# Kernel tuning notes

Measured on AMD Instinct MI355X. Metric: run time of the kernel, lower is better.

Reference implementation:

```python
import jax, jax.numpy as jnp
import numpy as np

NUM_CAPSULE = 16
DIM_CAPSULE = 64
ROUTINGS = 3
T_EPS = 1e-7


def setup_inputs() -> dict:
    key = jax.random.key(0)
    k1, k2 = jax.random.split(key)
    x = jax.random.normal(k1, (64, 512, 768), dtype=jnp.float32)
    # xavier-normal-ish init for W: [1, input_dim_capsule, num_capsule*dim_capsule]
    fan_in, fan_out = 768, NUM_CAPSULE * DIM_CAPSULE
    std = float(np.sqrt(2.0 / (fan_in + fan_out)))
    W = jax.random.normal(k2, (1, 768, NUM_CAPSULE * DIM_CAPSULE), dtype=jnp.float32) * std
    return {"x": x, "W": W}


def _squash(v, eps=T_EPS):
    # NOTE: this module's 'squash' is pure L2 normalization with eps, not the
    # classic (s^2/(1+s^2)) squash.
    s2 = jnp.sum(v * v, axis=-1, keepdims=True)
    return v / jnp.sqrt(s2 + eps)


def reference(x, W):
    B, In, _ = x.shape
    # u_hat: [B, In, num*dim] -> [B, num, In, dim]
    u = jnp.matmul(x, W).reshape(B, In, NUM_CAPSULE, DIM_CAPSULE).transpose(0, 2, 1, 3)
    b = jnp.zeros((B, NUM_CAPSULE, In), dtype=u.dtype)  # routing logits
    outputs = None
    for i in range(ROUTINGS):
        # torch code softmaxes over the num_capsule axis (after permute dance)
        c = jax.nn.softmax(b, axis=1)  # [B, num, In]
        outputs = _squash(jnp.einsum('bij,bijk->bik', c, u))  # [B, num, dim]
        if i < ROUTINGS - 1:
            b = jnp.einsum('bik,bijk->bij', outputs, u)  # [B, num, In]
    return outputs
```

## Files before the change

kernel.cpp:

```cpp
#include <hip/hip_runtime.h>
#include <hip/hip_bf16.h>
#include <stdint.h>

#define BATCH 64
#define IN_CAPS 512
#define NCAP 16
#define DCAP 64
#define GN (NCAP * DCAP)
#define GM (BATCH * IN_CAPS)
#define GK 768

typedef __bf16 bf16;
typedef __attribute__((ext_vector_type(8))) __bf16 bf16x8;
typedef __attribute__((ext_vector_type(4))) float f32x4;

__device__ inline void async16(const bf16* g, bf16* l) {
    __builtin_amdgcn_global_load_lds(
        (__attribute__((address_space(1))) void*)g,
        (__attribute__((address_space(3))) void*)l, 16, 0, 0);
}

__global__ __launch_bounds__(256) void k_convX2(const float* __restrict__ X,
                                                bf16* __restrict__ Xb,
                                                float* __restrict__ XS) {
    __shared__ float ls[GK];
    const int tid = threadIdx.x;
    ls[tid] = 0.f; ls[tid + 256] = 0.f; ls[tid + 512] = 0.f;
    __syncthreads();
    const size_t base = (size_t)blockIdx.x * (32 * GK);
    float acc[3][8] = {};
#pragma unroll
    for (int r = 0; r < 12; ++r) {
        const int off = r * 2048 + tid * 8;
        const f32x4 a0 = *(const f32x4*)(X + base + off);
        const f32x4 a1 = *(const f32x4*)(X + base + off + 4);
        bf16x8 o;
        o[0] = (bf16)a0[0]; o[1] = (bf16)a0[1]; o[2] = (bf16)a0[2]; o[3] = (bf16)a0[3];
        o[4] = (bf16)a1[0]; o[5] = (bf16)a1[1]; o[6] = (bf16)a1[2]; o[7] = (bf16)a1[3];
        *(bf16x8*)(Xb + base + off) = o;
        const int g = r % 3;
        acc[g][0] += a0[0]; acc[g][1] += a0[1];
        acc[g][2] += a0[2]; acc[g][3] += a0[3];
        acc[g][4] += a1[0]; acc[g][5] += a1[1];
        acc[g][6] += a1[2]; acc[g][7] += a1[3];
    }
    if (XS != nullptr) {
#pragma unroll
        for (int g = 0; g < 3; ++g) {
            const int cg = (g == 1) ? 512 : (g == 2) ? 256 : 0;
            const int kb = (tid * 8 + cg) % GK;
#pragma unroll
            for (int j = 0; j < 8; ++j) atomicAdd(&ls[kb + j], acc[g][j]);
        }
        __syncthreads();
        const int bidx = blockIdx.x >> 4;
        atomicAdd(&XS[(size_t)bidx * GK + tid],       ls[tid]);
        atomicAdd(&XS[(size_t)bidx * GK + tid + 256], ls[tid + 256]);
        atomicAdd(&XS[(size_t)bidx * GK + tid + 512], ls[tid + 512]);
    }
}

__global__ void k_transW(const float* __restrict__ W, bf16* __restrict__ Wt,
                         float* __restrict__ XS) {
    __shared__ bf16 t[32][33];
    const int k0 = blockIdx.x * 32;
    const int n0 = blockIdx.y * 32;
    const int tx = threadIdx.x, ty = threadIdx.y;
    if (XS != nullptr) {
        const int gid = (blockIdx.y * gridDim.x + blockIdx.x) * 256 + ty * 32 + tx;
        if (gid < BATCH * GK) XS[gid] = 0.f;
    }
#pragma unroll
    for (int r = 0; r < 4; ++r)
        t[ty + r * 8][tx] = (bf16)W[(size_t)(k0 + ty + r * 8) * GN + n0 + tx];
    __syncthreads();
#pragma unroll
    for (int r = 0; r < 4; ++r)
        Wt[(size_t)(n0 + ty + r * 8) * GK + k0 + tx] = t[tx][ty + r * 8];
}

__global__ __launch_bounds__(256) void k_out1(const float* __restrict__ XS,
                                              const float* __restrict__ W,
                                              float* __restrict__ O1) {
    __shared__ float xs[4][GK];
    __shared__ float red[4][4][64];
    const int cap = blockIdx.x & 15;
    const int bg = blockIdx.x >> 4;
    const int tid = threadIdx.x;
    const int k = tid & 63, kq = tid >> 6;
#pragma unroll
    for (int bb = 0; bb < 4; ++bb) {
        const size_t b = (size_t)(bg * 4 + bb);
        xs[bb][tid]       = XS[b * GK + tid];
        xs[bb][tid + 256] = XS[b * GK + tid + 256];
        xs[bb][tid + 512] = XS[b * GK + tid + 512];
    }
    __syncthreads();
    float acc4[4] = {0.f, 0.f, 0.f, 0.f};
    const float* wp = W + (size_t)(kq * 192) * GN + cap * 64 + k;
#pragma unroll 4
    for (int kk = 0; kk < 192; ++kk) {
        const float w = wp[(size_t)kk * GN];
        const int kx = kq * 192 + kk;
        acc4[0] += xs[0][kx] * w;
        acc4[1] += xs[1][kx] * w;
        acc4[2] += xs[2][kx] * w;
        acc4[3] += xs[3][kx] * w;
    }
#pragma unroll
    for (int bb = 0; bb < 4; ++bb) red[bb][kq][k] = acc4[bb];
    __syncthreads();
    if (tid < 64) {
#pragma unroll
        for (int bb = 0; bb < 4; ++bb) {
            float s = (red[bb][0][tid] + red[bb][1][tid] +
                       red[bb][2][tid] + red[bb][3][tid]) * 0.0625f;
            float ss = s * s;
#pragma unroll
            for (int off = 32; off >= 1; off >>= 1) ss += __shfl_xor(ss, off);
            O1[((size_t)(bg * 4 + bb) * NCAP + cap) * DCAP + tid] =
                s * rsqrtf(ss + 1e-7f);
        }
    }
}

__global__ __launch_bounds__(256) void k_gemm_pipe(const bf16* __restrict__ Xb,
                                                   const bf16* __restrict__ Wt,
                                                   const float* __restrict__ O1,
                                                   bf16* __restrict__ U,
                                                   float* __restrict__ BL) {
    __shared__ bf16 sA[3 * 4096];
    __shared__ bf16 sB[3 * 4096];

    const int tid = threadIdx.x;
    const int lane = tid & 63;
    const int wave = tid >> 6;
    const int wm = wave >> 1, wn = wave & 1;
    const int m0 = blockIdx.x * 128;
    const int n0 = blockIdx.y * 128;

    const int r16 = lane & 15, q8 = (lane >> 4) * 8;
    const bf16* gA0 = Xb + (size_t)(m0 + wave * 16 + r16) * GK + q8;
    const bf16* gA1 = Xb + (size_t)(m0 + (wave + 4) * 16 + r16) * GK + q8;
    const bf16* gB0 = Wt + (size_t)(n0 + wave * 16 + r16) * GK + q8;
    const bf16* gB1 = Wt + (size_t)(n0 + (wave + 4) * 16 + r16) * GK + q8;

    f32x4 acc[4][4] = {};

#define STAGE(BUF) do {                                        \
        async16(gA0, sA + (BUF) * 4096 + wave * 512);          \
        async16(gA1, sA + (BUF) * 4096 + (wave + 4) * 512);    \
        async16(gB0, sB + (BUF) * 4096 + wave * 512);          \
        async16(gB1, sB + (BUF) * 4096 + (wave + 4) * 512);    \
        gA0 += 32; gA1 += 32; gB0 += 32; gB1 += 32;            \
    } while (0)

    auto gstep = [&](int buf) {
        bf16x8 af[4], bv[4];
#pragma unroll
        for (int mi = 0; mi < 4; ++mi)
            af[mi] = *(const bf16x8*)(sA + buf * 4096 + (wm * 4 + mi) * 512 + lane * 8);
#pragma unroll
        for (int ni = 0; ni < 4; ++ni)
            bv[ni] = *(const bf16x8*)(sB + buf * 4096 + (wn * 4 + ni) * 512 + lane * 8);
#pragma unroll
        for (int mi = 0; mi < 4; ++mi)
#pragma unroll
            for (int ni = 0; ni < 4; ++ni)
                acc[mi][ni] = __builtin_amdgcn_mfma_f32_16x16x32_bf16(
                    af[mi], bv[ni], acc[mi][ni], 0, 0, 0);
    };

    STAGE(0);
    STAGE(1);

    int cur = 0, nxt = 2;
    for (int kt = 0; kt < GK / 32 - 2; ++kt) {
        asm volatile("s_waitcnt lgkmcnt(0)" ::: "memory");
        asm volatile("s_waitcnt vmcnt(4)" ::: "memory");
        __builtin_amdgcn_s_barrier();
        __builtin_amdgcn_sched_barrier(0);
        STAGE(nxt);
        gstep(cur);
        cur = (cur == 2) ? 0 : cur + 1;
        nxt = (nxt == 2) ? 0 : nxt + 1;
    }
    asm volatile("s_waitcnt lgkmcnt(0)" ::: "memory");
    asm volatile("s_waitcnt vmcnt(4)" ::: "memory");
    __builtin_amdgcn_s_barrier();
    __builtin_amdgcn_sched_barrier(0);
    gstep(1);
    asm volatile("s_waitcnt lgkmcnt(0)" ::: "memory");
    asm volatile("s_waitcnt vmcnt(0)" ::: "memory");
    __builtin_amdgcn_s_barrier();
    __builtin_amdgcn_sched_barrier(0);
    gstep(2);
#undef STAGE

    const int fr = lane & 15;
    const int fq = lane >> 4;
#pragma unroll
    for (int mi = 0; mi < 4; ++mi) {
#pragma unroll
        for (int ni = 0; ni < 4; ++ni) {
#pragma unroll
            for (int r = 0; r < 4; ++r) {
                const int m = m0 + wm * 64 + mi * 16 + fq * 4 + r;
                const int n = n0 + wn * 64 + ni * 16 + fr;
                const int bb = m >> 9, j = m & 511;
                const int ci = n >> 6, k = n & 63;
                U[(((size_t)(bb * NCAP + ci)) * IN_CAPS + j) * DCAP + k] =
                    (bf16)acc[mi][ni][r];
            }
        }
    }

    if (O1 != nullptr) {
        const int b = m0 >> 9;
        const int cap = (n0 >> 6) + wn;
        float o1v[4];
#pragma unroll
        for (int ni = 0; ni < 4; ++ni)
            o1v[ni] = O1[(size_t)b * GN + n0 + wn * 64 + ni * 16 + fr];
#pragma unroll
        for (int mi = 0; mi < 4; ++mi) {
#pragma unroll
            for (int r = 0; r < 4; ++r) {
                float p = o1v[0] * acc[mi][0][r] + o1v[1] * acc[mi][1][r] +
                          o1v[2] * acc[mi][2][r] + o1v[3] * acc[mi][3][r];
                p += __shfl_xor(p, 1);
                p += __shfl_xor(p, 2);
                p += __shfl_xor(p, 4);
                p += __shfl_xor(p, 8);
                if (fr == 0) {
                    const int j = (m0 & 511) + wm * 64 + mi * 16 + fq * 4 + r;
                    BL[((size_t)(b * NCAP + cap)) * IN_CAPS + j] = p;
                }
            }
        }
    }
}

__global__ __launch_bounds__(256) void k_gemm_inline(const float* __restrict__ X,
                                                     const bf16* __restrict__ Wt,
                                                     bf16* __restrict__ U) {
    __shared__ bf16 sA[128 * 32];
    __shared__ bf16 sB[128 * 32];
    const int tid = threadIdx.x;
    const int lane = tid & 63;
    const int wave = tid >> 6;
    const int wm = wave >> 1, wn = wave & 1;
    const int m0 = blockIdx.x * 128;
    const int n0 = blockIdx.y * 128;
    const int srow = tid >> 2;
    const int scol = (tid & 3) * 8;
    f32x4 acc[4][4] = {};
    const int fr = lane & 15;
    const int fq = lane >> 4;
    for (int kt = 0; kt < GK / 32; ++kt) {
        const int kb = kt * 32;
        bf16x8 a0, a1, b0, b1;
        {
            const float* p = X + (size_t)(m0 + srow) * GK + kb + scol;
            const f32x4 x0 = *(const f32x4*)p, x1 = *(const f32x4*)(p + 4);
            const float* q = X + (size_t)(m0 + srow + 64) * GK + kb + scol;
            const f32x4 y0 = *(const f32x4*)q, y1 = *(const f32x4*)(q + 4);
#pragma unroll
            for (int c = 0; c < 4; ++c) {
                a0[c] = (bf16)x0[c]; a0[c + 4] = (bf16)x1[c];
                a1[c] = (bf16)y0[c]; a1[c + 4] = (bf16)y1[c];
            }
        }
        b0 = *(const bf16x8*)(Wt + (size_t)(n0 + srow) * GK + kb + scol);
        b1 = *(const bf16x8*)(Wt + (size_t)(n0 + srow + 64) * GK + kb + scol);
        __syncthreads();
        *(bf16x8*)(sA + srow * 32 + scol) = a0;
        *(bf16x8*)(sA + (srow + 64) * 32 + scol) = a1;
        *(bf16x8*)(sB + srow * 32 + scol) = b0;
        *(bf16x8*)(sB + (srow + 64) * 32 + scol) = b1;
        __syncthreads();
        bf16x8 af[4], bfr[4];
#pragma unroll
        for (int mi = 0; mi < 4; ++mi)
            af[mi] = *(const bf16x8*)(sA + (wm * 64 + mi * 16 + fr) * 32 + fq * 8);
#pragma unroll
        for (int ni = 0; ni < 4; ++ni)
            bfr[ni] = *(const bf16x8*)(sB + (wn * 64 + ni * 16 + fr) * 32 + fq * 8);
#pragma unroll
        for (int mi = 0; mi < 4; ++mi)
#pragma unroll
            for (int ni = 0; ni < 4; ++ni)
                acc[mi][ni] = __builtin_amdgcn_mfma_f32_16x16x32_bf16(
                    af[mi], bfr[ni], acc[mi][ni], 0, 0, 0);
    }
#pragma unroll
    for (int mi = 0; mi < 4; ++mi) {
#pragma unroll
        for (int ni = 0; ni < 4; ++ni) {
#pragma unroll
            for (int r = 0; r < 4; ++r) {
                const int m = m0 + wm * 64 + mi * 16 + fq * 4 + r;
                const int n = n0 + wn * 64 + ni * 16 + fr;
                const int bb = m >> 9, j = m & 511;
                const int ci = n >> 6, k = n & 63;
                U[(((size_t)(bb * NCAP + ci)) * IN_CAPS + j) * DCAP + k] =
                    (bf16)acc[mi][ni][r];
            }
        }
    }
}

__global__ __launch_bounds__(256) void k_route(const bf16* __restrict__ U,
                                               float* __restrict__ BL,
                                               float* __restrict__ OutC,
                                               int mode) {
    __shared__ float sc[IN_CAPS];
    __shared__ float red[32][64];
    __shared__ float sout[64];
    const int bi = blockIdx.x;
    const int b = bi >> 4, cap = bi & 15;
    const int tid = threadIdx.x;
    const size_t ubase = (size_t)bi * IN_CAPS * DCAP;

    if (mode == 0) {
        sc[tid] = 0.0625f;
        sc[tid + 256] = 0.0625f;
    } else {
#pragma unroll
        for (int h = 0; h < 2; ++h) {
            const int j = tid + h * 256;
            const float* p = BL + (size_t)b * NCAP * IN_CAPS + j;
            float v[16], mx = -1e30f;
#pragma unroll
            for (int i = 0; i < 16; ++i) {
                v[i] = p[(size_t)i * IN_CAPS];
                mx = fmaxf(mx, v[i]);
            }
            float s = 0.f;
#pragma unroll
            for (int i = 0; i < 16; ++i) s += __expf(v[i] - mx);
            sc[j] = __expf(v[cap] - mx) / s;
        }
    }
    __syncthreads();

    const int g = tid & 7;
    const int jr = tid >> 3;

    float acc[8] = {};
#pragma unroll
    for (int it = 0; it < 16; ++it) {
        const int j = it * 32 + jr;
        const bf16x8 v = *(const bf16x8*)(U + ubase + (size_t)it * 2048 + tid * 8);
        const float cv = sc[j];
#pragma unroll
        for (int c = 0; c < 8; ++c) acc[c] += cv * (float)v[c];
    }
    *(f32x4*)(&red[jr][g * 8]) = f32x4{acc[0], acc[1], acc[2], acc[3]};
    *(f32x4*)(&red[jr][g * 8 + 4]) = f32x4{acc[4], acc[5], acc[6], acc[7]};
    __syncthreads();

    if (tid < 64) {
        float s = 0.f;
#pragma unroll
        for (int r = 0; r < 32; ++r) s += red[r][tid];
        float ss = s * s;
#pragma unroll
        for (int off = 32; off >= 1; off >>= 1) ss += __shfl_xor(ss, off);
        const float val = s * rsqrtf(ss + 1e-7f);
        sout[tid] = val;
        if (mode == 2) OutC[(size_t)bi * DCAP + tid] = val;
    }
    if (mode == 2) return;
    __syncthreads();

    const f32x4 o0 = *(const f32x4*)(sout + g * 8);
    const f32x4 o1 = *(const f32x4*)(sout + g * 8 + 4);
#pragma unroll
    for (int it = 0; it < 16; ++it) {
        const int j = it * 32 + jr;
        const bf16x8 v = *(const bf16x8*)(U + ubase + (size_t)it * 2048 + tid * 8);
        float p = o0[0] * (float)v[0] + o0[1] * (float)v[1] +
                  o0[2] * (float)v[2] + o0[3] * (float)v[3] +
                  o1[0] * (float)v[4] + o1[1] * (float)v[5] +
                  o1[2] * (float)v[6] + o1[3] * (float)v[7];
        p += __shfl_xor(p, 1);
        p += __shfl_xor(p, 2);
        p += __shfl_xor(p, 4);
        if (g == 0) BL[((size_t)b * NCAP + cap) * IN_CAPS + j] = p;
    }
}

extern "C" void kernel_launch(void* const* d_in, const int* in_sizes, int n_in,
                              void* d_out, int out_size, void* d_ws, size_t ws_size,
                              hipStream_t stream) {
    const float* X = (const float*)d_in[0];
    const float* W = (const float*)d_in[1];
    float* OutC = (float*)d_out;

    const size_t u_bytes = (size_t)BATCH * NCAP * IN_CAPS * DCAP * sizeof(bf16);
    const size_t xb_bytes = (size_t)GM * GK * sizeof(bf16);
    const size_t wt_bytes = (size_t)GN * GK * sizeof(bf16);
    const size_t bl_bytes = (size_t)BATCH * NCAP * IN_CAPS * sizeof(float);
    const size_t xs_bytes = (size_t)BATCH * GK * sizeof(float);
    const size_t o1_bytes = (size_t)BATCH * GN * sizeof(float);
    char* ws = (char*)d_ws;

    const size_t need_full = u_bytes + xb_bytes + wt_bytes + bl_bytes + xs_bytes + o1_bytes;
    const size_t need_async = u_bytes + xb_bytes + wt_bytes + bl_bytes;
    const size_t need_small = u_bytes + wt_bytes + bl_bytes;

    bf16* U = (bf16*)ws;

    if (ws_size >= need_full) {
        bf16* Xb = (bf16*)(ws + u_bytes);
        bf16* Wt = (bf16*)(ws + u_bytes + xb_bytes);
        float* BL = (float*)(ws + u_bytes + xb_bytes + wt_bytes);
        float* XS = (float*)(ws + u_bytes + xb_bytes + wt_bytes + bl_bytes);
        float* O1 = (float*)(ws + u_bytes + xb_bytes + wt_bytes + bl_bytes + xs_bytes);
        k_transW<<<dim3(GK / 32, GN / 32), dim3(32, 8), 0, stream>>>(W, Wt, XS);
        k_convX2<<<GM / 32, 256, 0, stream>>>(X, Xb, XS);
        k_out1<<<256, 256, 0, stream>>>(XS, W, O1);
        k_gemm_pipe<<<dim3(GM / 128, GN / 128), 256, 0, stream>>>(Xb, Wt, O1, U, BL);
        k_route<<<BATCH * NCAP, 256, 0, stream>>>(U, BL, OutC, 1);
        k_route<<<BATCH * NCAP, 256, 0, stream>>>(U, BL, OutC, 2);
    } else if (ws_size >= need_async) {
        bf16* Xb = (bf16*)(ws + u_bytes);
        bf16* Wt = (bf16*)(ws + u_bytes + xb_bytes);
        float* BL = (float*)(ws + u_bytes + xb_bytes + wt_bytes);
        k_transW<<<dim3(GK / 32, GN / 32), dim3(32, 8), 0, stream>>>(W, Wt, nullptr);
        k_convX2<<<GM / 32, 256, 0, stream>>>(X, Xb, nullptr);
        k_gemm_pipe<<<dim3(GM / 128, GN / 128), 256, 0, stream>>>(Xb, Wt, nullptr, U, BL);
        k_route<<<BATCH * NCAP, 256, 0, stream>>>(U, BL, OutC, 0);
        k_route<<<BATCH * NCAP, 256, 0, stream>>>(U, BL, OutC, 1);
        k_route<<<BATCH * NCAP, 256, 0, stream>>>(U, BL, OutC, 2);
    } else if (ws_size >= need_small) {
        bf16* Wt = (bf16*)(ws + u_bytes);
        float* BL = (float*)(ws + u_bytes + wt_bytes);
        k_transW<<<dim3(GK / 32, GN / 32), dim3(32, 8), 0, stream>>>(W, Wt, nullptr);
        k_gemm_inline<<<dim3(GM / 128, GN / 128), 256, 0, stream>>>(X, Wt, U);
        k_route<<<BATCH * NCAP, 256, 0, stream>>>(U, BL, OutC, 0);
        k_route<<<BATCH * NCAP, 256, 0, stream>>>(U, BL, OutC, 1);
        k_route<<<BATCH * NCAP, 256, 0, stream>>>(U, BL, OutC, 2);
    }
}
```

Baseline: 327.7 us.

## Drop GEMM triple buffering; cache U slice in LDS for routing logit pass

The GEMM main loop loses its three-stage async LDS pipeline and becomes a single-buffer loop with two barriers per K step. This shrinks LDS use but exposes global load latency. The routing kernel now stores its 64 KB U slice in shared memory during the first pass and rereads it from LDS for the logit pass instead of from global memory. Its reduction now uses wave shuffles plus a small 4x64 buffer instead of a 32x64 table. The 64 KB LDS footprint limits occupancy of the routing kernel.

```diff
diff --git a/kernel.cpp b/kernel.cpp
--- a/kernel.cpp
+++ b/kernel.cpp
@@ -124,13 +124,13 @@
     }
 }
 
-__global__ __launch_bounds__(256) void k_gemm_pipe(const bf16* __restrict__ Xb,
+__global__ __launch_bounds__(256) void k_gemm_frag(const bf16* __restrict__ Xb,
                                                    const bf16* __restrict__ Wt,
                                                    const float* __restrict__ O1,
                                                    bf16* __restrict__ U,
                                                    float* __restrict__ BL) {
-    __shared__ bf16 sA[3 * 4096];
-    __shared__ bf16 sB[3 * 4096];
+    __shared__ bf16 sA[4096];
+    __shared__ bf16 sB[4096];
 
     const int tid = threadIdx.x;
     const int lane = tid & 63;
@@ -147,55 +147,29 @@
 
     f32x4 acc[4][4] = {};
 
-#define STAGE(BUF) do {                                        \
-        async16(gA0, sA + (BUF) * 4096 + wave * 512);          \
-        async16(gA1, sA + (BUF) * 4096 + (wave + 4) * 512);    \
-        async16(gB0, sB + (BUF) * 4096 + wave * 512);          \
-        async16(gB1, sB + (BUF) * 4096 + (wave + 4) * 512);    \
-        gA0 += 32; gA1 += 32; gB0 += 32; gB1 += 32;            \
-    } while (0)
-
-    auto gstep = [&](int buf) {
+    for (int kt = 0; kt < GK / 32; ++kt) {
+        __syncthreads();
+        async16(gA0, sA + wave * 512);
+        async16(gA1, sA + (wave + 4) * 512);
+        async16(gB0, sB + wave * 512);
+        async16(gB1, sB + (wave + 4) * 512);
+        gA0 += 32; gA1 += 32; gB0 += 32; gB1 += 32;
+        __syncthreads();
+
         bf16x8 af[4], bv[4];
 #pragma unroll
         for (int mi = 0; mi < 4; ++mi)
-            af[mi] = *(const bf16x8*)(sA + buf * 4096 + (wm * 4 + mi) * 512 + lane * 8);
+            af[mi] = *(const bf16x8*)(sA + (wm * 4 + mi) * 512 + lane * 8);
 #pragma unroll
         for (int ni = 0; ni < 4; ++ni)
-            bv[ni] = *(const bf16x8*)(sB + buf * 4096 + (wn * 4 + ni) * 512 + lane * 8);
+            bv[ni] = *(const bf16x8*)(sB + (wn * 4 + ni) * 512 + lane * 8);
 #pragma unroll
         for (int mi = 0; mi < 4; ++mi)
 #pragma unroll
             for (int ni = 0; ni < 4; ++ni)
                 acc[mi][ni] = __builtin_amdgcn_mfma_f32_16x16x32_bf16(
                     af[mi], bv[ni], acc[mi][ni], 0, 0, 0);
-    };
-
-    STAGE(0);
-    STAGE(1);
-
-    int cur = 0, nxt = 2;
-    for (int kt = 0; kt < GK / 32 - 2; ++kt) {
-        asm volatile("s_waitcnt lgkmcnt(0)" ::: "memory");
-        asm volatile("s_waitcnt vmcnt(4)" ::: "memory");
-        __builtin_amdgcn_s_barrier();
-        __builtin_amdgcn_sched_barrier(0);
-        STAGE(nxt);
-        gstep(cur);
-        cur = (cur == 2) ? 0 : cur + 1;
-        nxt = (nxt == 2) ? 0 : nxt + 1;
-    }
-    asm volatile("s_waitcnt lgkmcnt(0)" ::: "memory");
-    asm volatile("s_waitcnt vmcnt(4)" ::: "memory");
-    __builtin_amdgcn_s_barrier();
-    __builtin_amdgcn_sched_barrier(0);
-    gstep(1);
-    asm volatile("s_waitcnt lgkmcnt(0)" ::: "memory");
-    asm volatile("s_waitcnt vmcnt(0)" ::: "memory");
-    __builtin_amdgcn_s_barrier();
-    __builtin_amdgcn_sched_barrier(0);
-    gstep(2);
-#undef STAGE
+    }
 
     const int fr = lane & 15;
     const int fq = lane >> 4;
@@ -314,12 +288,15 @@
                                                float* __restrict__ BL,
                                                float* __restrict__ OutC,
                                                int mode) {
+    __shared__ bf16 su[IN_CAPS * DCAP];
     __shared__ float sc[IN_CAPS];
-    __shared__ float red[32][64];
+    __shared__ float red2[4][64];
     __shared__ float sout[64];
     const int bi = blockIdx.x;
     const int b = bi >> 4, cap = bi & 15;
     const int tid = threadIdx.x;
+    const int lane = tid & 63;
+    const int wave = tid >> 6;
     const size_t ubase = (size_t)bi * IN_CAPS * DCAP;
 
     if (mode == 0) {
@@ -352,18 +329,25 @@
     for (int it = 0; it < 16; ++it) {
         const int j = it * 32 + jr;
         const bf16x8 v = *(const bf16x8*)(U + ubase + (size_t)it * 2048 + tid * 8);
+        if (mode != 2) *(bf16x8*)(su + it * 2048 + tid * 8) = v;
         const float cv = sc[j];
 #pragma unroll
         for (int c = 0; c < 8; ++c) acc[c] += cv * (float)v[c];
     }
-    *(f32x4*)(&red[jr][g * 8]) = f32x4{acc[0], acc[1], acc[2], acc[3]};
-    *(f32x4*)(&red[jr][g * 8 + 4]) = f32x4{acc[4], acc[5], acc[6], acc[7]};
+#pragma unroll
+    for (int c = 0; c < 8; ++c) {
+        acc[c] += __shfl_xor(acc[c], 8);
+        acc[c] += __shfl_xor(acc[c], 16);
+        acc[c] += __shfl_xor(acc[c], 32);
+    }
+    if ((lane >> 3) == 0) {
+#pragma unroll
+        for (int c = 0; c < 8; ++c) red2[wave][lane * 8 + c] = acc[c];
+    }
     __syncthreads();
 
     if (tid < 64) {
-        float s = 0.f;
-#pragma unroll
-        for (int r = 0; r < 32; ++r) s += red[r][tid];
+        float s = red2[0][tid] + red2[1][tid] + red2[2][tid] + red2[3][tid];
         float ss = s * s;
 #pragma unroll
         for (int off = 32; off >= 1; off >>= 1) ss += __shfl_xor(ss, off);
@@ -379,7 +363,7 @@
 #pragma unroll
     for (int it = 0; it < 16; ++it) {
         const int j = it * 32 + jr;
-        const bf16x8 v = *(const bf16x8*)(U + ubase + (size_t)it * 2048 + tid * 8);
+        const bf16x8 v = *(const bf16x8*)(su + it * 2048 + tid * 8);
         float p = o0[0] * (float)v[0] + o0[1] * (float)v[1] +
                   o0[2] * (float)v[2] + o0[3] * (float)v[3] +
                   o1[0] * (float)v[4] + o1[1] * (float)v[5] +
@@ -421,7 +405,7 @@
         k_transW<<<dim3(GK / 32, GN / 32), dim3(32, 8), 0, stream>>>(W, Wt, XS);
         k_convX2<<<GM / 32, 256, 0, stream>>>(X, Xb, XS);
         k_out1<<<256, 256, 0, stream>>>(XS, W, O1);
-        k_gemm_pipe<<<dim3(GM / 128, GN / 128), 256, 0, stream>>>(Xb, Wt, O1, U, BL);
+        k_gemm_frag<<<dim3(GM / 128, GN / 128), 256, 0, stream>>>(Xb, Wt, O1, U, BL);
         k_route<<<BATCH * NCAP, 256, 0, stream>>>(U, BL, OutC, 1);
         k_route<<<BATCH * NCAP, 256, 0, stream>>>(U, BL, OutC, 2);
     } else if (ws_size >= need_async) {
@@ -430,7 +414,7 @@
         float* BL = (float*)(ws + u_bytes + xb_bytes + wt_bytes);
         k_transW<<<dim3(GK / 32, GN / 32), dim3(32, 8), 0, stream>>>(W, Wt, nullptr);
         k_convX2<<<GM / 32, 256, 0, stream>>>(X, Xb, nullptr);
-        k_gemm_pipe<<<dim3(GM / 128, GN / 128), 256, 0, stream>>>(Xb, Wt, nullptr, U, BL);
+        k_gemm_frag<<<dim3(GM / 128, GN / 128), 256, 0, stream>>>(Xb, Wt, nullptr, U, BL);
         k_route<<<BATCH * NCAP, 256, 0, stream>>>(U, BL, OutC, 0);
         k_route<<<BATCH * NCAP, 256, 0, stream>>>(U, BL, OutC, 1);
         k_route<<<BATCH * NCAP, 256, 0, stream>>>(U, BL, OutC, 2);
```

Result: no change. 330.8 us (+0.9%).
